# Performance work log

Hardware: AMD Instinct MI355X
Metric: run time of the kernel (lower is better)

Reference implementation:

```python
import jax, jax.numpy as jnp
import numpy as np

B, H, S, D = 4, 16, 2048, 64

def setup_inputs() -> dict:
    key = jax.random.key(0)
    kq, kk, kv = jax.random.split(key, 3)
    Q = jax.random.normal(kq, (B, H, S, D), dtype=jnp.float32)
    K = jax.random.normal(kk, (B, H, S, D), dtype=jnp.float32)
    V = jax.random.normal(kv, (B, H, S, D), dtype=jnp.float32)
    return {"Q": Q, "K": K, "V": V}

def reference(Q, K, V):
    scale = K.shape[-1] ** -0.5
    # scores: [B, H, S, S]
    attn = jax.nn.softmax(jnp.einsum('bhqd,bhkd->bhqk', Q, K) * scale, axis=-1)
    # dropout is identity in eval/deterministic mode
    out = jnp.einsum('bhqk,bhkd->bhqd', attn, V)
    return out, attn
```

## Files before the change

### kernel.cpp

```cpp
#include <hip/hip_runtime.h>
#include <hip/hip_bf16.h>

#define SLEN 2048
#define DH   64
#define KT   64
#define NTL  32
#define NBH  64

typedef __attribute__((ext_vector_type(8))) short bf16x8;
typedef __attribute__((ext_vector_type(4))) short bf16x4;
typedef __attribute__((ext_vector_type(4))) float f32x4;

__device__ __forceinline__ short f2bf_hw(float f) {
    union { __hip_bfloat16 b; short s; } u;
    u.b = __float2bfloat16(f);
    return u.s;
}
__device__ __forceinline__ short2 f2bf2_hw(float a, float b) {
    union { __hip_bfloat162 b2; short2 s2; } u;
    u.b2 = __float22bfloat162_rn(float2{a, b});
    return u.s2;
}
__device__ __forceinline__ float bf2f(short s) {
    union { unsigned u; float f; } v;
    v.u = ((unsigned)(unsigned short)s) << 16;
    return v.f;
}

__device__ __forceinline__ short f2bf(float f) {
    union { float f; unsigned u; } v; v.f = f;
    unsigned u = v.u;
    u += 0x7fff + ((u >> 16) & 1);
    return (short)(u >> 16);
}

__global__ __launch_bounds__(256)
void conv_kernel(const float* __restrict__ K, const float* __restrict__ V,
                 short* __restrict__ Kw, short* __restrict__ Vt)
{
    __shared__ short lvt[DH][72];
    const int tid = threadIdx.x;
    const int blk = (int)blockIdx.x;
    const int bh = blk >> 5, t = blk & 31;
    const int r = tid >> 2;
    const int c = (tid & 3) << 4;

    if (blockIdx.y == 1) {
        const float4* src = (const float4*)(V + ((size_t)bh * SLEN + t * KT + r) * DH + c);
        #pragma unroll
        for (int q4 = 0; q4 < 4; ++q4) {
            float4 fv = src[q4];
            short2 p0 = f2bf2_hw(fv.x, fv.y);
            short2 p1 = f2bf2_hw(fv.z, fv.w);
            lvt[c + q4*4 + 0][r] = p0.x;
            lvt[c + q4*4 + 1][r] = p0.y;
            lvt[c + q4*4 + 2][r] = p1.x;
            lvt[c + q4*4 + 3][r] = p1.y;
        }
        __syncthreads();
        short* dst = Vt + (size_t)bh * DH * SLEN + (size_t)r * SLEN + t * KT + c;
        *(bf16x8*)dst       = *(const bf16x8*)&lvt[r][c];
        *(bf16x8*)(dst + 8) = *(const bf16x8*)&lvt[r][c + 8];
    } else {
        size_t off = ((size_t)bh * SLEN + t * KT + r) * DH + c;
        const float4* src = (const float4*)(K + off);
        alignas(16) short tmp[16];
        #pragma unroll
        for (int q4 = 0; q4 < 4; ++q4) {
            float4 fv = src[q4];
            *(short2*)&tmp[q4*4]     = f2bf2_hw(fv.x, fv.y);
            *(short2*)&tmp[q4*4 + 2] = f2bf2_hw(fv.z, fv.w);
        }
        *(bf16x8*)(Kw + off)     = *(const bf16x8*)&tmp[0];
        *(bf16x8*)(Kw + off + 8) = *(const bf16x8*)&tmp[8];
    }
}

__global__ __launch_bounds__(256, 3)
void sdpa_main(const float* __restrict__ Q, const short* __restrict__ Kw,
               const short* __restrict__ Vt, float* __restrict__ out,
               float* __restrict__ attn)
{
    __shared__ __align__(16) short lkv[4][KT][72];
    __shared__ __align__(16) short lp[4][16][72];

    const int tid = threadIdx.x;
    const int w = tid >> 6, lane = tid & 63, g = lane >> 4, lc = lane & 15;

    const int bid = (int)blockIdx.x;
    const int wg = (bid & 7) * 256 + (bid >> 3);
    const int qt = wg & 31, bh = wg >> 5;

    const short* Ktile = Kw + (size_t)bh * SLEN * DH;
    const short* Vbh   = Vt + (size_t)bh * DH * SLEN;
    float* outb  = out  + ((size_t)bh * SLEN + qt * KT) * DH;
    float* attnb = attn + ((size_t)bh * SLEN + qt * KT) * SLEN;

    const int srow = tid >> 3;
    const int scol = (tid & 7) * 8;

    const int rr = lane >> 4;
    const int cc = (lane & 15) * 4;

    bf16x8 qf[2];
    {
        const float* qsrc = Q + ((size_t)bh * SLEN + qt * KT + w * 16 + lc) * DH + g * 8;
        #pragma unroll
        for (int s = 0; s < 2; ++s)
            #pragma unroll
            for (int j = 0; j < 4; ++j) {
                short2 p = f2bf2_hw(qsrc[s * 32 + 2 * j] * 0.125f,
                                    qsrc[s * 32 + 2 * j + 1] * 0.125f);
                qf[s][2 * j]     = p.x;
                qf[s][2 * j + 1] = p.y;
            }
    }

    float lsum[4] = {0.f, 0.f, 0.f, 0.f};
    {
        #pragma unroll
        for (int p = 0; p < 2; ++p) {
            const short* ks = Ktile + p * (KT * DH);
            bf16x8 k0 = *(const bf16x8*)(ks + tid * 8);
            bf16x8 k1 = *(const bf16x8*)(ks + (tid + 256) * 8);
            *(bf16x8*)&lkv[p][srow][scol]      = k0;
            *(bf16x8*)&lkv[p][srow + 32][scol] = k1;
        }
    }
    __syncthreads();

    for (int t = 0; t < NTL; t += 2) {
        bf16x8 ka0, ka1, kb0, kb1;
        const bool pre = (t + 2 < NTL);
        if (pre) {
            const short* ksa = Ktile + (t + 2) * (KT * DH);
            const short* ksb = Ktile + (t + 3) * (KT * DH);
            ka0 = *(const bf16x8*)(ksa + tid * 8);
            ka1 = *(const bf16x8*)(ksa + (tid + 256) * 8);
            kb0 = *(const bf16x8*)(ksb + tid * 8);
            kb1 = *(const bf16x8*)(ksb + (tid + 256) * 8);
        }

        #pragma unroll
        for (int u = 0; u < 2; ++u) {
            const int slot = (t + u) & 3;
            f32x4 acc[4];
            #pragma unroll
            for (int nt = 0; nt < 4; ++nt) acc[nt] = (f32x4){0.f,0.f,0.f,0.f};
            #pragma unroll
            for (int s = 0; s < 2; ++s)
                #pragma unroll
                for (int nt = 0; nt < 4; ++nt) {
                    bf16x8 kf = *(const bf16x8*)&lkv[slot][nt * 16 + lc][s * 32 + g * 8];
                    acc[nt] = __builtin_amdgcn_mfma_f32_16x16x32_bf16(qf[s], kf, acc[nt], 0, 0, 0);
                }
            #pragma unroll
            for (int nt = 0; nt < 4; ++nt)
                #pragma unroll
                for (int e = 0; e < 4; ++e)
                    lsum[e] += __expf(acc[nt][e]);
        }

        if (pre) {
            *(bf16x8*)&lkv[(t + 2) & 3][srow][scol]      = ka0;
            *(bf16x8*)&lkv[(t + 2) & 3][srow + 32][scol] = ka1;
            *(bf16x8*)&lkv[(t + 3) & 3][srow][scol]      = kb0;
            *(bf16x8*)&lkv[(t + 3) & 3][srow + 32][scol] = kb1;
        }
        __syncthreads();
    }

    float c2[4];
    #pragma unroll
    for (int e = 0; e < 4; ++e) {
        float s = lsum[e];
        s += __shfl_xor(s, 1); s += __shfl_xor(s, 2);
        s += __shfl_xor(s, 4); s += __shfl_xor(s, 8);
        c2[e] = -__logf(s);
    }

    f32x4 oacc[4];
    #pragma unroll
    for (int nt = 0; nt < 4; ++nt) oacc[nt] = (f32x4){0.f,0.f,0.f,0.f};

    __syncthreads();
    {
        const short* ks = Ktile;
        const short* vs = Vbh;
        bf16x8 k0 = *(const bf16x8*)(ks + tid * 8);
        bf16x8 k1 = *(const bf16x8*)(ks + (tid + 256) * 8);
        bf16x8 v0 = *(const bf16x8*)(vs + (size_t)srow * SLEN + scol);
        bf16x8 v1 = *(const bf16x8*)(vs + (size_t)(srow + 32) * SLEN + scol);
        *(bf16x8*)&lkv[0][srow][scol]      = k0;
        *(bf16x8*)&lkv[0][srow + 32][scol] = k1;
        *(bf16x8*)&lkv[2][srow][scol]      = v0;
        *(bf16x8*)&lkv[2][srow + 32][scol] = v1;
    }
    __syncthreads();

    for (int t = 0; t < NTL; ++t) {
        bf16x8 k0, k1, v0, v1;
        const bool pre = (t + 1 < NTL);
        if (pre) {
            const short* ks = Ktile + (t + 1) * (KT * DH);
            const short* vs = Vbh + (t + 1) * KT;
            k0 = *(const bf16x8*)(ks + tid * 8);
            k1 = *(const bf16x8*)(ks + (tid + 256) * 8);
            v0 = *(const bf16x8*)(vs + (size_t)srow * SLEN + scol);
            v1 = *(const bf16x8*)(vs + (size_t)(srow + 32) * SLEN + scol);
        }

        f32x4 acc[4];
        #pragma unroll
        for (int nt = 0; nt < 4; ++nt) acc[nt] = (f32x4){0.f,0.f,0.f,0.f};
        #pragma unroll
        for (int s = 0; s < 2; ++s)
            #pragma unroll
            for (int nt = 0; nt < 4; ++nt) {
                bf16x8 kf = *(const bf16x8*)&lkv[t & 1][nt * 16 + lc][s * 32 + g * 8];
                acc[nt] = __builtin_amdgcn_mfma_f32_16x16x32_bf16(qf[s], kf, acc[nt], 0, 0, 0);
            }

        #pragma unroll
        for (int nt = 0; nt < 4; ++nt)
            #pragma unroll
            for (int e = 0; e < 4; ++e) {
                float p = __expf(acc[nt][e] + c2[e]);
                lp[w][4 * g + e][nt * 16 + lc] = f2bf_hw(p);
            }

        #pragma unroll
        for (int j = 0; j < 4; ++j) {
            const int row = j * 4 + rr;
            bf16x4 ps = *(const bf16x4*)&lp[w][row][cc];
            f32x4 qv = { bf2f(ps[0]), bf2f(ps[1]), bf2f(ps[2]), bf2f(ps[3]) };
            __builtin_nontemporal_store(
                qv, (f32x4*)(attnb + (size_t)(w * 16 + row) * SLEN + t * KT + cc));
        }

        #pragma unroll
        for (int kc = 0; kc < 2; ++kc) {
            bf16x8 pf = *(const bf16x8*)&lp[w][lc][kc * 32 + g * 8];
            #pragma unroll
            for (int nt = 0; nt < 4; ++nt) {
                bf16x8 vf = *(const bf16x8*)&lkv[2 + (t & 1)][nt * 16 + lc][kc * 32 + g * 8];
                oacc[nt] = __builtin_amdgcn_mfma_f32_16x16x32_bf16(pf, vf, oacc[nt], 0, 0, 0);
            }
        }

        if (pre) {
            *(bf16x8*)&lkv[(t + 1) & 1][srow][scol]      = k0;
            *(bf16x8*)&lkv[(t + 1) & 1][srow + 32][scol] = k1;
            *(bf16x8*)&lkv[2 + ((t + 1) & 1)][srow][scol]      = v0;
            *(bf16x8*)&lkv[2 + ((t + 1) & 1)][srow + 32][scol] = v1;
        }
        __syncthreads();
    }

    {
        float* lds_o = (float*)lkv;
        #pragma unroll
        for (int nt = 0; nt < 4; ++nt)
            #pragma unroll
            for (int e = 0; e < 4; ++e)
                lds_o[(w * 16 + 4 * g + e) * 72 + nt * 16 + lc] = oacc[nt][e];
        __syncthreads();
        #pragma unroll
        for (int j = 0; j < 4; ++j) {
            const int row = j * 16 + (tid >> 4);
            const int col = (tid & 15) * 4;
            f32x4 v = *(f32x4*)&lds_o[row * 72 + col];
            __builtin_nontemporal_store(v, (f32x4*)(outb + (size_t)row * DH + col));
        }
    }
}

__global__ __launch_bounds__(256, 3)
void sdpa_fallback(const float* __restrict__ Q, const float* __restrict__ K,
                   const float* __restrict__ V, float* __restrict__ out,
                   float* __restrict__ attn)
{
    __shared__ __align__(16) short lk[2][KT][72];
    __shared__ __align__(16) short lv[2][DH * 72];
    __shared__ __align__(16) short lp[4][16][72];

    const int tid = threadIdx.x;
    const int w = tid >> 6, lane = tid & 63, g = lane >> 4, lc = lane & 15;
    const int bid = (int)blockIdx.x;
    const int wg = (bid & 7) * 256 + (bid >> 3);
    const int qt = wg & 31, bh = wg >> 5;

    const float*  Qb  = Q + ((size_t)bh * SLEN + qt * 64) * DH;
    const float4* Kb4 = (const float4*)(K + (size_t)bh * SLEN * DH);
    const float4* Vb4 = (const float4*)(V + (size_t)bh * SLEN * DH);
    float* outb  = out  + ((size_t)bh * SLEN + qt * 64) * DH;
    float* attnb = attn + ((size_t)bh * SLEN + qt * 64) * SLEN;

    const int sr = (tid >> 4);
    const int sc = (tid & 15) * 4;

    bf16x8 qf[2];
    {
        const float* qsrc = Qb + (w * 16 + lc) * DH + g * 8;
        #pragma unroll
        for (int s = 0; s < 2; ++s)
            #pragma unroll
            for (int j = 0; j < 8; ++j)
                qf[s][j] = f2bf(qsrc[s * 32 + j] * 0.125f);
    }

    float lsum[4] = {0.f, 0.f, 0.f, 0.f};
    {
        float4 kr[4];
        #pragma unroll
        for (int q4 = 0; q4 < 4; ++q4) kr[q4] = Kb4[q4 * 256 + tid];
        #pragma unroll
        for (int q4 = 0; q4 < 4; ++q4) {
            short4 s4 = { f2bf(kr[q4].x), f2bf(kr[q4].y), f2bf(kr[q4].z), f2bf(kr[q4].w) };
            *(short4*)&lk[0][q4 * 16 + sr][sc] = s4;
        }
    }
    __syncthreads();
    for (int t = 0; t < NTL; ++t) {
        float4 kr[4];
        const bool pre = (t + 1 < NTL);
        if (pre) {
            const float4* src = Kb4 + (size_t)(t + 1) * 1024;
            #pragma unroll
            for (int q4 = 0; q4 < 4; ++q4) kr[q4] = src[q4 * 256 + tid];
        }
        f32x4 acc[4];
        #pragma unroll
        for (int nt = 0; nt < 4; ++nt) acc[nt] = (f32x4){0.f,0.f,0.f,0.f};
        #pragma unroll
        for (int s = 0; s < 2; ++s)
            #pragma unroll
            for (int nt = 0; nt < 4; ++nt) {
                bf16x8 kf = *(const bf16x8*)&lk[t & 1][nt * 16 + lc][s * 32 + g * 8];
                acc[nt] = __builtin_amdgcn_mfma_f32_16x16x32_bf16(qf[s], kf, acc[nt], 0, 0, 0);
            }
        #pragma unroll
        for (int nt = 0; nt < 4; ++nt)
            #pragma unroll
            for (int e = 0; e < 4; ++e)
                lsum[e] += __expf(acc[nt][e]);
        if (pre) {
            #pragma unroll
            for (int q4 = 0; q4 < 4; ++q4) {
                short4 s4 = { f2bf(kr[q4].x), f2bf(kr[q4].y), f2bf(kr[q4].z), f2bf(kr[q4].w) };
                *(short4*)&lk[(t + 1) & 1][q4 * 16 + sr][sc] = s4;
            }
        }
        __syncthreads();
    }
    float c2[4];
    #pragma unroll
    for (int e = 0; e < 4; ++e) {
        float s = lsum[e];
        s += __shfl_xor(s, 1); s += __shfl_xor(s, 2);
        s += __shfl_xor(s, 4); s += __shfl_xor(s, 8);
        c2[e] = -__logf(s);
    }
    f32x4 oacc[4];
    #pragma unroll
    for (int nt = 0; nt < 4; ++nt) oacc[nt] = (f32x4){0.f,0.f,0.f,0.f};
    {
        float4 kr[4], vr[4];
        #pragma unroll
        for (int q4 = 0; q4 < 4; ++q4) { kr[q4] = Kb4[q4 * 256 + tid]; vr[q4] = Vb4[q4 * 256 + tid]; }
        #pragma unroll
        for (int q4 = 0; q4 < 4; ++q4) {
            short4 s4 = { f2bf(kr[q4].x), f2bf(kr[q4].y), f2bf(kr[q4].z), f2bf(kr[q4].w) };
            *(short4*)&lk[0][q4 * 16 + sr][sc] = s4;
            float fv[4] = { vr[q4].x, vr[q4].y, vr[q4].z, vr[q4].w };
            #pragma unroll
            for (int j = 0; j < 4; ++j) {
                int d = sc + j;
                int idx = (d * 72 + q4 * 16 + sr) ^ (((d >> 3) & 7) << 3);
                lv[0][idx] = f2bf(fv[j]);
            }
        }
    }
    __syncthreads();
    for (int t = 0; t < NTL; ++t) {
        float4 kr[4], vr[4];
        const bool pre = (t + 1 < NTL);
        if (pre) {
            const float4* ks = Kb4 + (size_t)(t + 1) * 1024;
            const float4* vs = Vb4 + (size_t)(t + 1) * 1024;
            #pragma unroll
            for (int q4 = 0; q4 < 4; ++q4) { kr[q4] = ks[q4 * 256 + tid]; vr[q4] = vs[q4 * 256 + tid]; }
        }
        f32x4 acc[4];
        #pragma unroll
        for (int nt = 0; nt < 4; ++nt) acc[nt] = (f32x4){0.f,0.f,0.f,0.f};
        #pragma unroll
        for (int s = 0; s < 2; ++s)
            #pragma unroll
            for (int nt = 0; nt < 4; ++nt) {
                bf16x8 kf = *(const bf16x8*)&lk[t & 1][nt * 16 + lc][s * 32 + g * 8];
                acc[nt] = __builtin_amdgcn_mfma_f32_16x16x32_bf16(qf[s], kf, acc[nt], 0, 0, 0);
            }
        #pragma unroll
        for (int nt = 0; nt < 4; ++nt)
            #pragma unroll
            for (int e = 0; e < 4; ++e) {
                float p = __expf(acc[nt][e] + c2[e]);
                attnb[(size_t)(w * 16 + 4 * g + e) * SLEN + t * KT + nt * 16 + lc] = p;
                lp[w][4 * g + e][nt * 16 + lc] = f2bf(p);
            }
        const short* lvb = lv[t & 1];
        #pragma unroll
        for (int kc = 0; kc < 2; ++kc) {
            bf16x8 pf = *(const bf16x8*)&lp[w][lc][kc * 32 + g * 8];
            #pragma unroll
            for (int nt = 0; nt < 4; ++nt) {
                int d0 = nt * 16 + lc;
                int idx = (d0 * 72 + kc * 32 + g * 8) ^ (((d0 >> 3) & 7) << 3);
                bf16x8 vfrag = *(const bf16x8*)&lvb[idx];
                oacc[nt] = __builtin_amdgcn_mfma_f32_16x16x32_bf16(pf, vfrag, oacc[nt], 0, 0, 0);
            }
        }
        if (pre) {
            #pragma unroll
            for (int q4 = 0; q4 < 4; ++q4) {
                short4 s4 = { f2bf(kr[q4].x), f2bf(kr[q4].y), f2bf(kr[q4].z), f2bf(kr[q4].w) };
                *(short4*)&lk[(t + 1) & 1][q4 * 16 + sr][sc] = s4;
                float fv[4] = { vr[q4].x, vr[q4].y, vr[q4].z, vr[q4].w };
                #pragma unroll
                for (int j = 0; j < 4; ++j) {
                    int d = sc + j;
                    int idx = (d * 72 + q4 * 16 + sr) ^ (((d >> 3) & 7) << 3);
                    lv[(t + 1) & 1][idx] = f2bf(fv[j]);
                }
            }
        }
        __syncthreads();
    }
    #pragma unroll
    for (int nt = 0; nt < 4; ++nt)
        #pragma unroll
        for (int e = 0; e < 4; ++e)
            outb[(w * 16 + 4 * g + e) * DH + nt * 16 + lc] = oacc[nt][e];
}

extern "C" void kernel_launch(void* const* d_in, const int* in_sizes, int n_in,
                              void* d_out, int out_size, void* d_ws, size_t ws_size,
                              hipStream_t stream) {
    const float* Q = (const float*)d_in[0];
    const float* K = (const float*)d_in[1];
    const float* V = (const float*)d_in[2];
    float* out  = (float*)d_out;
    float* attn = out + (size_t)NBH * SLEN * DH;

    const size_t nelem = (size_t)NBH * SLEN * DH;
    if (ws_size >= 2 * nelem * sizeof(short)) {
        short* Kw = (short*)d_ws;
        short* Vt = Kw + nelem;
        conv_kernel<<<dim3(2048, 2), dim3(256), 0, stream>>>(K, V, Kw, Vt);
        sdpa_main<<<dim3(2048), dim3(256), 0, stream>>>(Q, Kw, Vt, out, attn);
    } else {
        sdpa_fallback<<<dim3(2048), dim3(256), 0, stream>>>(Q, K, V, out, attn);
    }
}
```

Baseline: 247.6 us.

## Fuse K/V bf16 conversion into a softmax-denominator first pass kernel

```diff
diff --git a/kernel.cpp b/kernel.cpp
--- a/kernel.cpp
+++ b/kernel.cpp
@@ -34,19 +34,30 @@
     return (short)(u >> 16);
 }
 
-__global__ __launch_bounds__(256)
-void conv_kernel(const float* __restrict__ K, const float* __restrict__ V,
-                 short* __restrict__ Kw, short* __restrict__ Vt)
+__global__ __launch_bounds__(256, 3)
+void pass1_kernel(const float* __restrict__ Q, const float* __restrict__ K,
+                  const float* __restrict__ V,
+                  short* __restrict__ Kw, short* __restrict__ Vt,
+                  float* __restrict__ c2g)
 {
-    __shared__ short lvt[DH][72];
+    __shared__ __align__(16) short lk[2][KT][72];
+    __shared__ __align__(16) short lvt[KT][72];
+
     const int tid = threadIdx.x;
-    const int blk = (int)blockIdx.x;
-    const int bh = blk >> 5, t = blk & 31;
+    const int w = tid >> 6, lane = tid & 63, g = lane >> 4, lc = lane & 15;
+
+    const int bid = (int)blockIdx.x;
+    const int wg = (bid & 7) * 256 + (bid >> 3);
+    const int qt = wg & 31, bh = wg >> 5;
+
     const int r = tid >> 2;
     const int c = (tid & 3) << 4;
 
-    if (blockIdx.y == 1) {
-        const float4* src = (const float4*)(V + ((size_t)bh * SLEN + t * KT + r) * DH + c);
+    const float* Kbh = K + (size_t)bh * SLEN * DH;
+    short* Kwp = Kw + (size_t)bh * SLEN * DH;
+
+    {
+        const float4* src = (const float4*)(V + ((size_t)bh * SLEN + qt * KT + r) * DH + c);
         #pragma unroll
         for (int q4 = 0; q4 < 4; ++q4) {
             float4 fv = src[q4];
@@ -58,49 +69,10 @@
             lvt[c + q4*4 + 3][r] = p1.y;
         }
         __syncthreads();
-        short* dst = Vt + (size_t)bh * DH * SLEN + (size_t)r * SLEN + t * KT + c;
+        short* dst = Vt + (size_t)bh * DH * SLEN + (size_t)r * SLEN + qt * KT + c;
         *(bf16x8*)dst       = *(const bf16x8*)&lvt[r][c];
         *(bf16x8*)(dst + 8) = *(const bf16x8*)&lvt[r][c + 8];
-    } else {
-        size_t off = ((size_t)bh * SLEN + t * KT + r) * DH + c;
-        const float4* src = (const float4*)(K + off);
-        alignas(16) short tmp[16];
-        #pragma unroll
-        for (int q4 = 0; q4 < 4; ++q4) {
-            float4 fv = src[q4];
-            *(short2*)&tmp[q4*4]     = f2bf2_hw(fv.x, fv.y);
-            *(short2*)&tmp[q4*4 + 2] = f2bf2_hw(fv.z, fv.w);
-        }
-        *(bf16x8*)(Kw + off)     = *(const bf16x8*)&tmp[0];
-        *(bf16x8*)(Kw + off + 8) = *(const bf16x8*)&tmp[8];
-    }
-}
-
-__global__ __launch_bounds__(256, 3)
-void sdpa_main(const float* __restrict__ Q, const short* __restrict__ Kw,
-               const short* __restrict__ Vt, float* __restrict__ out,
-               float* __restrict__ attn)
-{
-    __shared__ __align__(16) short lkv[4][KT][72];
-    __shared__ __align__(16) short lp[4][16][72];
-
-    const int tid = threadIdx.x;
-    const int w = tid >> 6, lane = tid & 63, g = lane >> 4, lc = lane & 15;
-
-    const int bid = (int)blockIdx.x;
-    const int wg = (bid & 7) * 256 + (bid >> 3);
-    const int qt = wg & 31, bh = wg >> 5;
-
-    const short* Ktile = Kw + (size_t)bh * SLEN * DH;
-    const short* Vbh   = Vt + (size_t)bh * DH * SLEN;
-    float* outb  = out  + ((size_t)bh * SLEN + qt * KT) * DH;
-    float* attnb = attn + ((size_t)bh * SLEN + qt * KT) * SLEN;
-
-    const int srow = tid >> 3;
-    const int scol = (tid & 7) * 8;
-
-    const int rr = lane >> 4;
-    const int cc = (lane & 15) * 4;
+    }
 
     bf16x8 qf[2];
     {
@@ -118,72 +90,122 @@
 
     float lsum[4] = {0.f, 0.f, 0.f, 0.f};
     {
-        #pragma unroll
-        for (int p = 0; p < 2; ++p) {
-            const short* ks = Ktile + p * (KT * DH);
-            bf16x8 k0 = *(const bf16x8*)(ks + tid * 8);
-            bf16x8 k1 = *(const bf16x8*)(ks + (tid + 256) * 8);
-            *(bf16x8*)&lkv[p][srow][scol]      = k0;
-            *(bf16x8*)&lkv[p][srow + 32][scol] = k1;
-        }
+        const float4* src = (const float4*)(Kbh + (size_t)r * DH + c);
+        alignas(16) short tmp[16];
+        #pragma unroll
+        for (int q4 = 0; q4 < 4; ++q4) {
+            float4 fv = src[q4];
+            *(short2*)&tmp[q4*4]     = f2bf2_hw(fv.x, fv.y);
+            *(short2*)&tmp[q4*4 + 2] = f2bf2_hw(fv.z, fv.w);
+        }
+        *(bf16x8*)&lk[0][r][c]     = *(const bf16x8*)&tmp[0];
+        *(bf16x8*)&lk[0][r][c + 8] = *(const bf16x8*)&tmp[8];
     }
     __syncthreads();
 
-    for (int t = 0; t < NTL; t += 2) {
-        bf16x8 ka0, ka1, kb0, kb1;
-        const bool pre = (t + 2 < NTL);
-        if (pre) {
-            const short* ksa = Ktile + (t + 2) * (KT * DH);
-            const short* ksb = Ktile + (t + 3) * (KT * DH);
-            ka0 = *(const bf16x8*)(ksa + tid * 8);
-            ka1 = *(const bf16x8*)(ksa + (tid + 256) * 8);
-            kb0 = *(const bf16x8*)(ksb + tid * 8);
-            kb1 = *(const bf16x8*)(ksb + (tid + 256) * 8);
-        }
-
-        #pragma unroll
-        for (int u = 0; u < 2; ++u) {
-            const int slot = (t + u) & 3;
-            f32x4 acc[4];
-            #pragma unroll
-            for (int nt = 0; nt < 4; ++nt) acc[nt] = (f32x4){0.f,0.f,0.f,0.f};
-            #pragma unroll
-            for (int s = 0; s < 2; ++s)
-                #pragma unroll
-                for (int nt = 0; nt < 4; ++nt) {
-                    bf16x8 kf = *(const bf16x8*)&lkv[slot][nt * 16 + lc][s * 32 + g * 8];
-                    acc[nt] = __builtin_amdgcn_mfma_f32_16x16x32_bf16(qf[s], kf, acc[nt], 0, 0, 0);
-                }
-            #pragma unroll
-            for (int nt = 0; nt < 4; ++nt)
-                #pragma unroll
-                for (int e = 0; e < 4; ++e)
-                    lsum[e] += __expf(acc[nt][e]);
-        }
-
-        if (pre) {
-            *(bf16x8*)&lkv[(t + 2) & 3][srow][scol]      = ka0;
-            *(bf16x8*)&lkv[(t + 2) & 3][srow + 32][scol] = ka1;
-            *(bf16x8*)&lkv[(t + 3) & 3][srow][scol]      = kb0;
-            *(bf16x8*)&lkv[(t + 3) & 3][srow + 32][scol] = kb1;
-        }
-        __syncthreads();
-    }
-
-    float c2[4];
+    for (int t = 0; t < NTL; ++t) {
+        float4 kr[4];
+        const bool pre = (t + 1 < NTL);
+        if (pre) {
+            const float4* src = (const float4*)(Kbh + (size_t)((t + 1) * KT + r) * DH + c);
+            #pragma unroll
+            for (int q4 = 0; q4 < 4; ++q4) kr[q4] = src[q4];
+        }
+
+        f32x4 acc[4];
+        #pragma unroll
+        for (int nt = 0; nt < 4; ++nt) acc[nt] = (f32x4){0.f,0.f,0.f,0.f};
+        #pragma unroll
+        for (int s = 0; s < 2; ++s)
+            #pragma unroll
+            for (int nt = 0; nt < 4; ++nt) {
+                bf16x8 kf = *(const bf16x8*)&lk[t & 1][nt * 16 + lc][s * 32 + g * 8];
+                acc[nt] = __builtin_amdgcn_mfma_f32_16x16x32_bf16(qf[s], kf, acc[nt], 0, 0, 0);
+            }
+        #pragma unroll
+        for (int nt = 0; nt < 4; ++nt)
+            #pragma unroll
+            for (int e = 0; e < 4; ++e)
+                lsum[e] += __expf(acc[nt][e]);
+
+        if (t == qt) {
+            bf16x8 a  = *(const bf16x8*)&lk[t & 1][r][c];
+            bf16x8 b2 = *(const bf16x8*)&lk[t & 1][r][c + 8];
+            short* kd = Kwp + t * (KT * DH) + r * DH + c;
+            *(bf16x8*)kd       = a;
+            *(bf16x8*)(kd + 8) = b2;
+        }
+
+        if (pre) {
+            alignas(16) short tmp[16];
+            #pragma unroll
+            for (int q4 = 0; q4 < 4; ++q4) {
+                float4 fv = kr[q4];
+                *(short2*)&tmp[q4*4]     = f2bf2_hw(fv.x, fv.y);
+                *(short2*)&tmp[q4*4 + 2] = f2bf2_hw(fv.z, fv.w);
+            }
+            *(bf16x8*)&lk[(t + 1) & 1][r][c]     = *(const bf16x8*)&tmp[0];
+            *(bf16x8*)&lk[(t + 1) & 1][r][c + 8] = *(const bf16x8*)&tmp[8];
+        }
+        __syncthreads();
+    }
+
     #pragma unroll
     for (int e = 0; e < 4; ++e) {
         float s = lsum[e];
         s += __shfl_xor(s, 1); s += __shfl_xor(s, 2);
         s += __shfl_xor(s, 4); s += __shfl_xor(s, 8);
-        c2[e] = -__logf(s);
+        if (lc == 0)
+            c2g[(size_t)wg * 64 + w * 16 + 4 * g + e] = -__logf(s);
+    }
+}
+
+__global__ __launch_bounds__(256, 3)
+void pass2_kernel(const float* __restrict__ Q, const short* __restrict__ Kw,
+                  const short* __restrict__ Vt, const float* __restrict__ c2g,
+                  float* __restrict__ out, float* __restrict__ attn)
+{
+    __shared__ __align__(16) short lkv[4][KT][72];
+    __shared__ __align__(16) short lp[4][16][72];
+    __shared__ float lc2[64];
+
+    const int tid = threadIdx.x;
+    const int w = tid >> 6, lane = tid & 63, g = lane >> 4, lc = lane & 15;
+
+    const int bid = (int)blockIdx.x;
+    const int wg = (bid & 7) * 256 + (bid >> 3);
+    const int qt = wg & 31, bh = wg >> 5;
+
+    const short* Ktile = Kw + (size_t)bh * SLEN * DH;
+    const short* Vbh   = Vt + (size_t)bh * DH * SLEN;
+    float* outb  = out  + ((size_t)bh * SLEN + qt * KT) * DH;
+    float* attnb = attn + ((size_t)bh * SLEN + qt * KT) * SLEN;
+
+    const int srow = tid >> 3;
+    const int scol = (tid & 7) * 8;
+    const int rr = lane >> 4;
+    const int cc = (lane & 15) * 4;
+
+    if (tid < 64) lc2[tid] = c2g[(size_t)wg * 64 + tid];
+
+    bf16x8 qf[2];
+    {
+        const float* qsrc = Q + ((size_t)bh * SLEN + qt * KT + w * 16 + lc) * DH + g * 8;
+        #pragma unroll
+        for (int s = 0; s < 2; ++s)
+            #pragma unroll
+            for (int j = 0; j < 4; ++j) {
+                short2 p = f2bf2_hw(qsrc[s * 32 + 2 * j] * 0.125f,
+                                    qsrc[s * 32 + 2 * j + 1] * 0.125f);
+                qf[s][2 * j]     = p.x;
+                qf[s][2 * j + 1] = p.y;
+            }
     }
 
     f32x4 oacc[4];
     #pragma unroll
     for (int nt = 0; nt < 4; ++nt) oacc[nt] = (f32x4){0.f,0.f,0.f,0.f};
 
-    __syncthreads();
     {
         const short* ks = Ktile;
         const short* vs = Vbh;
@@ -198,6 +220,10 @@
     }
     __syncthreads();
 
+    float c2[4];
+    #pragma unroll
+    for (int e = 0; e < 4; ++e) c2[e] = lc2[w * 16 + 4 * g + e];
+
     for (int t = 0; t < NTL; ++t) {
         bf16x8 k0, k1, v0, v1;
         const bool pre = (t + 1 < NTL);
@@ -454,11 +480,13 @@
     float* attn = out + (size_t)NBH * SLEN * DH;
 
     const size_t nelem = (size_t)NBH * SLEN * DH;
-    if (ws_size >= 2 * nelem * sizeof(short)) {
+    const size_t need = 2 * nelem * sizeof(short) + (size_t)2048 * 64 * sizeof(float);
+    if (ws_size >= need) {
         short* Kw = (short*)d_ws;
         short* Vt = Kw + nelem;
-        conv_kernel<<<dim3(2048, 2), dim3(256), 0, stream>>>(K, V, Kw, Vt);
-        sdpa_main<<<dim3(2048), dim3(256), 0, stream>>>(Q, Kw, Vt, out, attn);
+        float* c2g = (float*)(Vt + nelem);
+        pass1_kernel<<<dim3(2048), dim3(256), 0, stream>>>(Q, K, V, Kw, Vt, c2g);
+        pass2_kernel<<<dim3(2048), dim3(256), 0, stream>>>(Q, Kw, Vt, c2g, out, attn);
     } else {
         sdpa_fallback<<<dim3(2048), dim3(256), 0, stream>>>(Q, K, V, out, attn);
     }
```

Measured after the change: 294.9 us. 1.19x slower.
